# Kernel optimization log

Measured on AMD Instinct MI355X. Metric: run time of the kernel, lower is better.

Reference implementation:

```python
import jax, jax.numpy as jnp
from jax import lax
import numpy as np

SLOPE = 0.1  # LeakyReLU negative slope used throughout DA_conv


def setup_inputs() -> dict:
    key = jax.random.key(0)
    ks = jax.random.split(key, 8)
    B, C, H, W = 16, 64, 160, 160
    Cout, red = 64, 8
    feat = jax.random.normal(ks[0], (B, C, H, W), dtype=jnp.float32)
    deg = jax.random.normal(ks[1], (B, C, 1, 1), dtype=jnp.float32)
    W1 = jax.random.normal(ks[2], (64, C), dtype=jnp.float32) * 0.05
    W2 = jax.random.normal(ks[3], (Cout * 9, 64), dtype=jnp.float32) * 0.05
    Wc = jax.random.normal(ks[4], (Cout, Cout), dtype=jnp.float32) * 0.05
    bc = jnp.zeros((Cout,), dtype=jnp.float32)
    Wd1 = jax.random.normal(ks[5], (red, C), dtype=jnp.float32) * 0.05
    Wd2 = jax.random.normal(ks[6], (Cout, red), dtype=jnp.float32) * 0.05
    return {"feat": feat, "deg": deg, "W1": W1, "W2": W2, "Wc": Wc,
            "bc": bc, "Wd1": Wd1, "Wd2": Wd2}


def reference(feat, deg, W1, W2, Wc, bc, Wd1, Wd2):
    B, C, H, W = feat.shape
    Cout = Wc.shape[0]
    KS = 3
    d = deg[:, :, 0, 0]  # [B, C]

    # --- dynamic per-sample, per-channel 3x3 kernel generation ---
    h = jax.nn.leaky_relu(d @ W1.T, SLOPE)            # [B, 64]
    k = (h @ W2.T).reshape(B * Cout, 1, KS, KS)        # [B*Cout, 1, 3, 3]

    # grouped depthwise conv: input [1, B*C, H, W], groups = B*C
    x = feat.reshape(1, B * C, H, W)
    out = lax.conv_general_dilated(
        x, k, window_strides=(1, 1), padding=[(1, 1), (1, 1)],
        dimension_numbers=("NCHW", "OIHW", "NCHW"),
        feature_group_count=B * C)
    out = jax.nn.leaky_relu(out, SLOPE).reshape(B, Cout, H, W)

    # 1x1 conv with bias (common.default_conv)
    out = jnp.einsum("oi,bihw->bohw", Wc, out) + bc[None, :, None, None]

    # --- channel attention branch (1x1 convs == matmuls on [B,C]) ---
    a = jax.nn.leaky_relu(jnp.einsum("ri,bi->br", Wd1, d), SLOPE)   # [B, red]
    att = jax.nn.sigmoid(jnp.einsum("or,br->bo", Wd2, a))           # [B, Cout]

    return out + feat * att[:, :, None, None]
```

## Files before the change

### kernel.cpp

```cpp
#include <hip/hip_runtime.h>
#include <hip/hip_bf16.h>
#include <math.h>

#define SLOPE 0.1f
#define B_ 16
#define C_ 64
#define H_ 160
#define W_ 160
#define HW_ (H_*W_)

typedef short bf16x8 __attribute__((ext_vector_type(8)));
typedef float f32x4  __attribute__((ext_vector_type(4)));
typedef unsigned int uint2v __attribute__((ext_vector_type(2)));

__device__ __forceinline__ float lrelu(float x) { return fmaxf(x, SLOPE * x); }
__device__ __forceinline__ unsigned f2bf(float x) {
  union { float f; unsigned u; } c; c.f = x;
  return (c.u + 0x7fffu + ((c.u >> 16) & 1u)) >> 16;
}
__device__ __forceinline__ float bf2f(unsigned short u) {
  union { unsigned u; float f; } c; c.u = ((unsigned)u) << 16; return c.f;
}

__device__ __forceinline__ void gl2lds16(const void* g, void* l) {
  __builtin_amdgcn_global_load_lds(
      (const __attribute__((address_space(1))) void*)g,
      (__attribute__((address_space(3))) void*)l, 16, 0, 0);
}

__global__ __launch_bounds__(64) void prep_kernel(
    const float* __restrict__ deg,
    const float* __restrict__ W1,
    const float* __restrict__ W2,
    const float* __restrict__ Wd1,
    const float* __restrict__ Wd2,
    float* __restrict__ ws) {
  const int b = blockIdx.x;
  const int j = threadIdx.x;
  __shared__ float sd[64], sh[64], sa[8];
  sd[j] = deg[b * 64 + j];
  __syncthreads();

  float acc = 0.f;
  for (int i = 0; i < 64; ++i) acc = fmaf(sd[i], W1[j * 64 + i], acc);
  sh[j] = lrelu(acc);

  if (j < 8) {
    float s = 0.f;
    for (int i = 0; i < 64; ++i) s = fmaf(sd[i], Wd1[j * 64 + i], s);
    sa[j] = lrelu(s);
  }
  __syncthreads();

  float kv[9];
#pragma unroll
  for (int t = 0; t < 9; ++t) kv[t] = 0.f;
  for (int l = 0; l < 64; ++l) {
    float hl = sh[l];
#pragma unroll
    for (int t = 0; t < 9; ++t) kv[t] = fmaf(hl, W2[(j * 9 + t) * 64 + l], kv[t]);
  }
  unsigned short* kw = (unsigned short*)(ws + 1024) + (b * 64 + j) * 16;
#pragma unroll
  for (int t = 0; t < 9; ++t) kw[t] = (unsigned short)f2bf(kv[t]);
#pragma unroll
  for (int t = 9; t < 16; ++t) kw[t] = 0;

  float s2 = 0.f;
#pragma unroll
  for (int r = 0; r < 8; ++r) s2 = fmaf(Wd2[j * 8 + r], sa[r], s2);
  ws[b * 64 + j] = 1.f / (1.f + __expf(-s2));
}

__global__ __launch_bounds__(256, 4) void main_kernel(
    const float* __restrict__ feat,
    const float* __restrict__ Wc,
    const float* __restrict__ bc,
    const float* __restrict__ ws,
    float* __restrict__ out) {
  __shared__ __align__(16) float S[2][16][240];
  __shared__ __align__(16) unsigned short Tt[2048];
  __shared__ __align__(16) unsigned short Ff[2048];
  __shared__ __align__(16) unsigned short Kl[1024];

  const int rb  = blockIdx.x;
  const int bid = (rb & 7) * 400 + (rb >> 3);
  const int b   = bid / 200;
  const int rem = bid - b * 200;
  const int ty  = rem / 10, tx = rem - ty * 10;
  const int x0 = tx * 16, y0 = ty * 8;
  const int tid = threadIdx.x;
  const int lane = tid & 63, wid = tid >> 6;

  const float* __restrict__ attp  = ws + b * 64;
  const char*  __restrict__ kb8   = (const char*)(ws + 1024) + b * 2048;
  const float* __restrict__ plane = feat + (size_t)(b * 64) * HW_;

  const int ci = tid >> 4;
  const int q  = (tid >> 2) & 3;
  const int h  = tid & 3;
  const int nl = lane & 15, kg = lane >> 4;
  const int ochunk = wid * 16;

  const int srow = lane / 6;
  const int schk = lane - srow * 6;
  const int grow = min(max(y0 + srow - 1, 0), H_ - 1);
  const int gcol = min(max(x0 - 4 + schk * 4, 0), W_ - 4);
  const float* sp0 = plane + grow * W_ + gcol;

  union AF { bf16x8 v; unsigned short u[8]; };
  AF a[4];
#pragma unroll
  for (int g = 0; g < 4; ++g) {
    const float4 w = *(const float4*)(Wc + (ochunk + nl) * 64 + g * 16 + 4 * kg);
    a[g].u[0] = (unsigned short)f2bf(w.x); a[g].u[1] = (unsigned short)f2bf(w.y);
    a[g].u[2] = (unsigned short)f2bf(w.z); a[g].u[3] = (unsigned short)f2bf(w.w);
    a[g].u[4] = 0; a[g].u[5] = 0; a[g].u[6] = 0; a[g].u[7] = 0;
  }
  AF a2;
  {
    const unsigned short ab = (unsigned short)f2bf(attp[ochunk + nl]);
#pragma unroll
    for (int j = 0; j < 4; ++j) a2.u[j] = (nl == 4 * kg + j) ? ab : (unsigned short)0;
    a2.u[4] = 0; a2.u[5] = 0; a2.u[6] = 0; a2.u[7] = 0;
  }
  const float4 bcv = *(const float4*)(bc + ochunk + 4 * kg);

  asm volatile("s_waitcnt vmcnt(0)" ::: "memory");

  if (wid == 0) {
    gl2lds16(kb8 + lane * 16, &Kl[0]);
    gl2lds16(kb8 + 1024 + lane * 16, &Kl[512]);
  }
#define STAGE(g_, bf_) \
  if (lane < 60) { \
    const float* s_ = sp0 + (size_t)((g_) * 16 + wid * 4) * HW_; \
    gl2lds16(s_,            &S[bf_][wid * 4 + 0][0]); \
    gl2lds16(s_ + HW_,      &S[bf_][wid * 4 + 1][0]); \
    gl2lds16(s_ + 2 * HW_,  &S[bf_][wid * 4 + 2][0]); \
    gl2lds16(s_ + 3 * HW_,  &S[bf_][wid * 4 + 3][0]); \
  }
  STAGE(0, 0);
  asm volatile("s_waitcnt vmcnt(4)" ::: "memory");
  __builtin_amdgcn_s_barrier();
  __builtin_amdgcn_sched_barrier(0);

  f32x4 acc[8];
#pragma unroll
  for (int nt = 0; nt < 8; ++nt) acc[nt] = (f32x4){0.f, 0.f, 0.f, 0.f};

  const float mlz = (x0 == 0 && q == 0) ? 0.f : 1.f;
  const float mrz = (x0 == W_ - 16 && q == 3) ? 0.f : 1.f;

  const unsigned t_base = (unsigned)(uintptr_t)&Tt[0] + (unsigned)(lane * 8);
  const unsigned f_base = (unsigned)(uintptr_t)&Ff[0] + (unsigned)(lane * 8);
  union BU { bf16x8 v; uint2v qv[2]; };

#pragma unroll
  for (int g = 0; g < 4; ++g) {
    const int sb = g & 1;
    if (g < 3) {
      STAGE(g + 1, (g + 1) & 1);
      asm volatile("s_waitcnt vmcnt(4)" ::: "memory");
    } else {
      asm volatile("s_waitcnt vmcnt(0)" ::: "memory");
    }
    __builtin_amdgcn_sched_barrier(0);

    const unsigned short* kr = &Kl[(g * 16 + ci) * 16];
    union KU { uint4 v; unsigned short u[8]; } k07;
    k07.v = *(const uint4*)kr;
    const unsigned short k8u = kr[8];
    float kk[9];
#pragma unroll
    for (int t = 0; t < 8; ++t) kk[t] = bf2f(k07.u[t]);
    kk[8] = bf2f(k8u);

    float rv[4][9];
#pragma unroll
    for (int rr = 0; rr < 4; ++rr) {
      const float* sp = &S[sb][ci][(2 * h + rr) * 24 + 4 * q];
      const f32x4 v0 = *(const f32x4*)sp;
      const f32x4 v1 = *(const f32x4*)(sp + 4);
      rv[rr][0] = v0[0]; rv[rr][1] = v0[1]; rv[rr][2] = v0[2];
      rv[rr][3] = v0[3] * mlz;
      rv[rr][4] = v1[0]; rv[rr][5] = v1[1]; rv[rr][6] = v1[2]; rv[rr][7] = v1[3];
      rv[rr][8] = sp[8] * mrz;
    }

#pragma unroll
    for (int rr = 0; rr < 2; ++rr) {
      const int srw = 2 * h + rr;
      const float mt = (srw == 0 && y0 == 0) ? 0.f : 1.f;
      const float mb = (srw == 7 && y0 == H_ - 8) ? 0.f : 1.f;
      float sv[4], fv[4];
#pragma unroll
      for (int j = 0; j < 4; ++j) {
        float ts = fmaf(rv[rr][j + 5], kk[2], fmaf(rv[rr][j + 4], kk[1], rv[rr][j + 3] * kk[0]));
        float cs = fmaf(rv[rr + 1][j + 5], kk[5], fmaf(rv[rr + 1][j + 4], kk[4], rv[rr + 1][j + 3] * kk[3]));
        float bs = fmaf(rv[rr + 2][j + 5], kk[8], fmaf(rv[rr + 2][j + 4], kk[7], rv[rr + 2][j + 3] * kk[6]));
        sv[j] = fmaf(mt, ts, fmaf(mb, bs, cs));
        fv[j] = rv[rr + 1][j + 4];
      }
      uint2v tq, fq;
      tq.x = f2bf(lrelu(sv[0])) | (f2bf(lrelu(sv[1])) << 16);
      tq.y = f2bf(lrelu(sv[2])) | (f2bf(lrelu(sv[3])) << 16);
      fq.x = f2bf(fv[0]) | (f2bf(fv[1]) << 16);
      fq.y = f2bf(fv[2]) | (f2bf(fv[3]) << 16);
      const int tidx = srw * 256 + ci * 16 + 4 * q;
      *(uint2v*)&Tt[tidx] = tq;
      *(uint2v*)&Ff[tidx] = fq;
    }

    asm volatile("s_waitcnt lgkmcnt(0)" ::: "memory");
    __builtin_amdgcn_sched_barrier(0);
    __builtin_amdgcn_s_barrier();
    __builtin_amdgcn_sched_barrier(0);

    uint2v ta0, ta1, ta2, ta3, tb0, tb1, tb2, tb3;
    asm volatile("ds_read_b64_tr_b16 %0, %1 offset:0"    : "=v"(ta0) : "v"(t_base));
    asm volatile("ds_read_b64_tr_b16 %0, %1 offset:512"  : "=v"(ta1) : "v"(t_base));
    asm volatile("ds_read_b64_tr_b16 %0, %1 offset:1024" : "=v"(ta2) : "v"(t_base));
    asm volatile("ds_read_b64_tr_b16 %0, %1 offset:1536" : "=v"(ta3) : "v"(t_base));
    asm volatile("s_waitcnt lgkmcnt(0)" ::: "memory");
    __builtin_amdgcn_sched_barrier(0);
    asm volatile("ds_read_b64_tr_b16 %0, %1 offset:2048" : "=v"(tb0) : "v"(t_base));
    asm volatile("ds_read_b64_tr_b16 %0, %1 offset:2560" : "=v"(tb1) : "v"(t_base));
    asm volatile("ds_read_b64_tr_b16 %0, %1 offset:3072" : "=v"(tb2) : "v"(t_base));
    asm volatile("ds_read_b64_tr_b16 %0, %1 offset:3584" : "=v"(tb3) : "v"(t_base));
    {
      BU u0, u1, u2, u3;
      u0.qv[0] = ta0; u0.qv[1] = (uint2v){0u, 0u};
      u1.qv[0] = ta1; u1.qv[1] = (uint2v){0u, 0u};
      u2.qv[0] = ta2; u2.qv[1] = (uint2v){0u, 0u};
      u3.qv[0] = ta3; u3.qv[1] = (uint2v){0u, 0u};
      acc[0] = __builtin_amdgcn_mfma_f32_16x16x32_bf16(a[g].v, u0.v, acc[0], 0, 0, 0);
      acc[1] = __builtin_amdgcn_mfma_f32_16x16x32_bf16(a[g].v, u1.v, acc[1], 0, 0, 0);
      acc[2] = __builtin_amdgcn_mfma_f32_16x16x32_bf16(a[g].v, u2.v, acc[2], 0, 0, 0);
      acc[3] = __builtin_amdgcn_mfma_f32_16x16x32_bf16(a[g].v, u3.v, acc[3], 0, 0, 0);
    }
    asm volatile("s_waitcnt lgkmcnt(0)" ::: "memory");
    __builtin_amdgcn_sched_barrier(0);
    {
      BU u4, u5, u6, u7;
      u4.qv[0] = tb0; u4.qv[1] = (uint2v){0u, 0u};
      u5.qv[0] = tb1; u5.qv[1] = (uint2v){0u, 0u};
      u6.qv[0] = tb2; u6.qv[1] = (uint2v){0u, 0u};
      u7.qv[0] = tb3; u7.qv[1] = (uint2v){0u, 0u};
      acc[4] = __builtin_amdgcn_mfma_f32_16x16x32_bf16(a[g].v, u4.v, acc[4], 0, 0, 0);
      acc[5] = __builtin_amdgcn_mfma_f32_16x16x32_bf16(a[g].v, u5.v, acc[5], 0, 0, 0);
      acc[6] = __builtin_amdgcn_mfma_f32_16x16x32_bf16(a[g].v, u6.v, acc[6], 0, 0, 0);
      acc[7] = __builtin_amdgcn_mfma_f32_16x16x32_bf16(a[g].v, u7.v, acc[7], 0, 0, 0);
    }
    if (wid == g) {
      uint2v fa0, fa1, fa2, fa3, fb0, fb1, fb2, fb3;
      asm volatile("ds_read_b64_tr_b16 %0, %1 offset:0"    : "=v"(fa0) : "v"(f_base));
      asm volatile("ds_read_b64_tr_b16 %0, %1 offset:512"  : "=v"(fa1) : "v"(f_base));
      asm volatile("ds_read_b64_tr_b16 %0, %1 offset:1024" : "=v"(fa2) : "v"(f_base));
      asm volatile("ds_read_b64_tr_b16 %0, %1 offset:1536" : "=v"(fa3) : "v"(f_base));
      asm volatile("s_waitcnt lgkmcnt(0)" ::: "memory");
      __builtin_amdgcn_sched_barrier(0);
      asm volatile("ds_read_b64_tr_b16 %0, %1 offset:2048" : "=v"(fb0) : "v"(f_base));
      asm volatile("ds_read_b64_tr_b16 %0, %1 offset:2560" : "=v"(fb1) : "v"(f_base));
      asm volatile("ds_read_b64_tr_b16 %0, %1 offset:3072" : "=v"(fb2) : "v"(f_base));
      asm volatile("ds_read_b64_tr_b16 %0, %1 offset:3584" : "=v"(fb3) : "v"(f_base));
      {
        BU u0, u1, u2, u3;
        u0.qv[0] = fa0; u0.qv[1] = (uint2v){0u, 0u};
        u1.qv[0] = fa1; u1.qv[1] = (uint2v){0u, 0u};
        u2.qv[0] = fa2; u2.qv[1] = (uint2v){0u, 0u};
        u3.qv[0] = fa3; u3.qv[1] = (uint2v){0u, 0u};
        acc[0] = __builtin_amdgcn_mfma_f32_16x16x32_bf16(a2.v, u0.v, acc[0], 0, 0, 0);
        acc[1] = __builtin_amdgcn_mfma_f32_16x16x32_bf16(a2.v, u1.v, acc[1], 0, 0, 0);
        acc[2] = __builtin_amdgcn_mfma_f32_16x16x32_bf16(a2.v, u2.v, acc[2], 0, 0, 0);
        acc[3] = __builtin_amdgcn_mfma_f32_16x16x32_bf16(a2.v, u3.v, acc[3], 0, 0, 0);
      }
      asm volatile("s_waitcnt lgkmcnt(0)" ::: "memory");
      __builtin_amdgcn_sched_barrier(0);
      {
        BU u4, u5, u6, u7;
        u4.qv[0] = fb0; u4.qv[1] = (uint2v){0u, 0u};
        u5.qv[0] = fb1; u5.qv[1] = (uint2v){0u, 0u};
        u6.qv[0] = fb2; u6.qv[1] = (uint2v){0u, 0u};
        u7.qv[0] = fb3; u7.qv[1] = (uint2v){0u, 0u};
        acc[4] = __builtin_amdgcn_mfma_f32_16x16x32_bf16(a2.v, u4.v, acc[4], 0, 0, 0);
        acc[5] = __builtin_amdgcn_mfma_f32_16x16x32_bf16(a2.v, u5.v, acc[5], 0, 0, 0);
        acc[6] = __builtin_amdgcn_mfma_f32_16x16x32_bf16(a2.v, u6.v, acc[6], 0, 0, 0);
        acc[7] = __builtin_amdgcn_mfma_f32_16x16x32_bf16(a2.v, u7.v, acc[7], 0, 0, 0);
      }
    }
    __builtin_amdgcn_s_barrier();
    __builtin_amdgcn_sched_barrier(0);
  }
#undef STAGE

  const int ob = ochunk + 4 * kg;
  float* __restrict__ outb = out + (size_t)(b * 64) * HW_;
#pragma unroll
  for (int nt = 0; nt < 8; ++nt) {
    const int off = (y0 + nt) * W_ + x0 + nl;
    outb[(size_t)(ob + 0) * HW_ + off] = acc[nt][0] + bcv.x;
    outb[(size_t)(ob + 1) * HW_ + off] = acc[nt][1] + bcv.y;
    outb[(size_t)(ob + 2) * HW_ + off] = acc[nt][2] + bcv.z;
    outb[(size_t)(ob + 3) * HW_ + off] = acc[nt][3] + bcv.w;
  }
}

extern "C" void kernel_launch(void* const* d_in, const int* in_sizes, int n_in,
                              void* d_out, int out_size, void* d_ws, size_t ws_size,
                              hipStream_t stream) {
  const float* feat = (const float*)d_in[0];
  const float* deg  = (const float*)d_in[1];
  const float* W1   = (const float*)d_in[2];
  const float* W2   = (const float*)d_in[3];
  const float* Wc   = (const float*)d_in[4];
  const float* bc   = (const float*)d_in[5];
  const float* Wd1  = (const float*)d_in[6];
  const float* Wd2  = (const float*)d_in[7];
  float* out = (float*)d_out;
  float* ws  = (float*)d_ws;

  prep_kernel<<<dim3(B_), dim3(64), 0, stream>>>(deg, W1, W2, Wd1, Wd2, ws);
  main_kernel<<<dim3(3200), dim3(256), 0, stream>>>(feat, Wc, bc, ws, out);
}
```

Baseline: 67.30 us.

## Fold attention MFMA into main MFMA K-slot and deepen staging pipeline

Packs the attention-diagonal A fragment into the unused upper K half of each Wc fragment. The wave that owns the attention term for a group now issues one set of 8 MFMAs combining conv output and feature, not 16. Input staging is restructured so two groups are prefetched up front and the next-next group is issued after the LDS writes, removing the initial barrier. Dynamic-kernel weights are stored in a permuted slot order so all four waves load them cooperatively. This adds a tighter dependency between buffer reuse and the barrier, and interleaved ds_read waits.

```diff
diff --git a/kernel.cpp b/kernel.cpp
--- a/kernel.cpp
+++ b/kernel.cpp
@@ -60,7 +60,8 @@
 #pragma unroll
     for (int t = 0; t < 9; ++t) kv[t] = fmaf(hl, W2[(j * 9 + t) * 64 + l], kv[t]);
   }
-  unsigned short* kw = (unsigned short*)(ws + 1024) + (b * 64 + j) * 16;
+  const int slot = ((j & 15) >> 2) * 16 + (j >> 4) * 4 + (j & 3);
+  unsigned short* kw = (unsigned short*)(ws + 1024) + (b * 64 + slot) * 16;
 #pragma unroll
   for (int t = 0; t < 9; ++t) kw[t] = (unsigned short)f2bf(kv[t]);
 #pragma unroll
@@ -110,28 +111,21 @@
 
   union AF { bf16x8 v; unsigned short u[8]; };
   AF a[4];
+  const unsigned short ab = (unsigned short)f2bf(attp[ochunk + nl]);
 #pragma unroll
   for (int g = 0; g < 4; ++g) {
     const float4 w = *(const float4*)(Wc + (ochunk + nl) * 64 + g * 16 + 4 * kg);
     a[g].u[0] = (unsigned short)f2bf(w.x); a[g].u[1] = (unsigned short)f2bf(w.y);
     a[g].u[2] = (unsigned short)f2bf(w.z); a[g].u[3] = (unsigned short)f2bf(w.w);
-    a[g].u[4] = 0; a[g].u[5] = 0; a[g].u[6] = 0; a[g].u[7] = 0;
-  }
-  AF a2;
-  {
-    const unsigned short ab = (unsigned short)f2bf(attp[ochunk + nl]);
-#pragma unroll
-    for (int j = 0; j < 4; ++j) a2.u[j] = (nl == 4 * kg + j) ? ab : (unsigned short)0;
-    a2.u[4] = 0; a2.u[5] = 0; a2.u[6] = 0; a2.u[7] = 0;
+#pragma unroll
+    for (int j = 0; j < 4; ++j)
+      a[g].u[4 + j] = (wid == g && nl == 4 * kg + j) ? ab : (unsigned short)0;
   }
   const float4 bcv = *(const float4*)(bc + ochunk + 4 * kg);
 
   asm volatile("s_waitcnt vmcnt(0)" ::: "memory");
 
-  if (wid == 0) {
-    gl2lds16(kb8 + lane * 16, &Kl[0]);
-    gl2lds16(kb8 + 1024 + lane * 16, &Kl[512]);
-  }
+  if (lane < 32) gl2lds16(kb8 + wid * 512 + lane * 16, &Kl[wid * 256]);
 #define STAGE(g_, bf_) \
   if (lane < 60) { \
     const float* s_ = sp0 + (size_t)((g_) * 16 + wid * 4) * HW_; \
@@ -141,9 +135,7 @@
     gl2lds16(s_ + 3 * HW_,  &S[bf_][wid * 4 + 3][0]); \
   }
   STAGE(0, 0);
-  asm volatile("s_waitcnt vmcnt(4)" ::: "memory");
-  __builtin_amdgcn_s_barrier();
-  __builtin_amdgcn_sched_barrier(0);
+  STAGE(1, 1);
 
   f32x4 acc[8];
 #pragma unroll
@@ -160,14 +152,13 @@
   for (int g = 0; g < 4; ++g) {
     const int sb = g & 1;
     if (g < 3) {
-      STAGE(g + 1, (g + 1) & 1);
       asm volatile("s_waitcnt vmcnt(4)" ::: "memory");
     } else {
       asm volatile("s_waitcnt vmcnt(0)" ::: "memory");
     }
     __builtin_amdgcn_sched_barrier(0);
 
-    const unsigned short* kr = &Kl[(g * 16 + ci) * 16];
+    const unsigned short* kr = &Kl[(wid * 16 + g * 4 + (lane >> 4)) * 16];
     union KU { uint4 v; unsigned short u[8]; } k07;
     k07.v = *(const uint4*)kr;
     const unsigned short k8u = kr[8];
@@ -212,81 +203,103 @@
       *(uint2v*)&Ff[tidx] = fq;
     }
 
+    if (g < 2) { STAGE(g + 2, sb); }
+
     asm volatile("s_waitcnt lgkmcnt(0)" ::: "memory");
     __builtin_amdgcn_sched_barrier(0);
     __builtin_amdgcn_s_barrier();
     __builtin_amdgcn_sched_barrier(0);
 
-    uint2v ta0, ta1, ta2, ta3, tb0, tb1, tb2, tb3;
-    asm volatile("ds_read_b64_tr_b16 %0, %1 offset:0"    : "=v"(ta0) : "v"(t_base));
-    asm volatile("ds_read_b64_tr_b16 %0, %1 offset:512"  : "=v"(ta1) : "v"(t_base));
-    asm volatile("ds_read_b64_tr_b16 %0, %1 offset:1024" : "=v"(ta2) : "v"(t_base));
-    asm volatile("ds_read_b64_tr_b16 %0, %1 offset:1536" : "=v"(ta3) : "v"(t_base));
-    asm volatile("s_waitcnt lgkmcnt(0)" ::: "memory");
-    __builtin_amdgcn_sched_barrier(0);
-    asm volatile("ds_read_b64_tr_b16 %0, %1 offset:2048" : "=v"(tb0) : "v"(t_base));
-    asm volatile("ds_read_b64_tr_b16 %0, %1 offset:2560" : "=v"(tb1) : "v"(t_base));
-    asm volatile("ds_read_b64_tr_b16 %0, %1 offset:3072" : "=v"(tb2) : "v"(t_base));
-    asm volatile("ds_read_b64_tr_b16 %0, %1 offset:3584" : "=v"(tb3) : "v"(t_base));
-    {
-      BU u0, u1, u2, u3;
-      u0.qv[0] = ta0; u0.qv[1] = (uint2v){0u, 0u};
-      u1.qv[0] = ta1; u1.qv[1] = (uint2v){0u, 0u};
-      u2.qv[0] = ta2; u2.qv[1] = (uint2v){0u, 0u};
-      u3.qv[0] = ta3; u3.qv[1] = (uint2v){0u, 0u};
-      acc[0] = __builtin_amdgcn_mfma_f32_16x16x32_bf16(a[g].v, u0.v, acc[0], 0, 0, 0);
-      acc[1] = __builtin_amdgcn_mfma_f32_16x16x32_bf16(a[g].v, u1.v, acc[1], 0, 0, 0);
-      acc[2] = __builtin_amdgcn_mfma_f32_16x16x32_bf16(a[g].v, u2.v, acc[2], 0, 0, 0);
-      acc[3] = __builtin_amdgcn_mfma_f32_16x16x32_bf16(a[g].v, u3.v, acc[3], 0, 0, 0);
-    }
-    asm volatile("s_waitcnt lgkmcnt(0)" ::: "memory");
-    __builtin_amdgcn_sched_barrier(0);
-    {
-      BU u4, u5, u6, u7;
-      u4.qv[0] = tb0; u4.qv[1] = (uint2v){0u, 0u};
-      u5.qv[0] = tb1; u5.qv[1] = (uint2v){0u, 0u};
-      u6.qv[0] = tb2; u6.qv[1] = (uint2v){0u, 0u};
-      u7.qv[0] = tb3; u7.qv[1] = (uint2v){0u, 0u};
-      acc[4] = __builtin_amdgcn_mfma_f32_16x16x32_bf16(a[g].v, u4.v, acc[4], 0, 0, 0);
-      acc[5] = __builtin_amdgcn_mfma_f32_16x16x32_bf16(a[g].v, u5.v, acc[5], 0, 0, 0);
-      acc[6] = __builtin_amdgcn_mfma_f32_16x16x32_bf16(a[g].v, u6.v, acc[6], 0, 0, 0);
-      acc[7] = __builtin_amdgcn_mfma_f32_16x16x32_bf16(a[g].v, u7.v, acc[7], 0, 0, 0);
-    }
     if (wid == g) {
-      uint2v fa0, fa1, fa2, fa3, fb0, fb1, fb2, fb3;
-      asm volatile("ds_read_b64_tr_b16 %0, %1 offset:0"    : "=v"(fa0) : "v"(f_base));
-      asm volatile("ds_read_b64_tr_b16 %0, %1 offset:512"  : "=v"(fa1) : "v"(f_base));
-      asm volatile("ds_read_b64_tr_b16 %0, %1 offset:1024" : "=v"(fa2) : "v"(f_base));
-      asm volatile("ds_read_b64_tr_b16 %0, %1 offset:1536" : "=v"(fa3) : "v"(f_base));
+      uint2v t0, t1, t2, t3, t4, t5, t6, t7;
+      uint2v f0, f1, f2, f3, f4, f5, f6, f7;
+      asm volatile("ds_read_b64_tr_b16 %0, %1 offset:0"    : "=v"(t0) : "v"(t_base));
+      asm volatile("ds_read_b64_tr_b16 %0, %1 offset:512"  : "=v"(t1) : "v"(t_base));
+      asm volatile("ds_read_b64_tr_b16 %0, %1 offset:0"    : "=v"(f0) : "v"(f_base));
+      asm volatile("ds_read_b64_tr_b16 %0, %1 offset:512"  : "=v"(f1) : "v"(f_base));
+      asm volatile("ds_read_b64_tr_b16 %0, %1 offset:1024" : "=v"(t2) : "v"(t_base));
+      asm volatile("ds_read_b64_tr_b16 %0, %1 offset:1536" : "=v"(t3) : "v"(t_base));
+      asm volatile("ds_read_b64_tr_b16 %0, %1 offset:1024" : "=v"(f2) : "v"(f_base));
+      asm volatile("ds_read_b64_tr_b16 %0, %1 offset:1536" : "=v"(f3) : "v"(f_base));
+      asm volatile("s_waitcnt lgkmcnt(4)" ::: "memory");
+      __builtin_amdgcn_sched_barrier(0);
+      {
+        BU u0, u1;
+        u0.qv[0] = t0; u0.qv[1] = f0;
+        u1.qv[0] = t1; u1.qv[1] = f1;
+        acc[0] = __builtin_amdgcn_mfma_f32_16x16x32_bf16(a[g].v, u0.v, acc[0], 0, 0, 0);
+        acc[1] = __builtin_amdgcn_mfma_f32_16x16x32_bf16(a[g].v, u1.v, acc[1], 0, 0, 0);
+      }
+      asm volatile("ds_read_b64_tr_b16 %0, %1 offset:2048" : "=v"(t4) : "v"(t_base));
+      asm volatile("ds_read_b64_tr_b16 %0, %1 offset:2560" : "=v"(t5) : "v"(t_base));
+      asm volatile("ds_read_b64_tr_b16 %0, %1 offset:2048" : "=v"(f4) : "v"(f_base));
+      asm volatile("ds_read_b64_tr_b16 %0, %1 offset:2560" : "=v"(f5) : "v"(f_base));
+      asm volatile("s_waitcnt lgkmcnt(4)" ::: "memory");
+      __builtin_amdgcn_sched_barrier(0);
+      {
+        BU u2, u3;
+        u2.qv[0] = t2; u2.qv[1] = f2;
+        u3.qv[0] = t3; u3.qv[1] = f3;
+        acc[2] = __builtin_amdgcn_mfma_f32_16x16x32_bf16(a[g].v, u2.v, acc[2], 0, 0, 0);
+        acc[3] = __builtin_amdgcn_mfma_f32_16x16x32_bf16(a[g].v, u3.v, acc[3], 0, 0, 0);
+      }
+      asm volatile("ds_read_b64_tr_b16 %0, %1 offset:3072" : "=v"(t6) : "v"(t_base));
+      asm volatile("ds_read_b64_tr_b16 %0, %1 offset:3584" : "=v"(t7) : "v"(t_base));
+      asm volatile("ds_read_b64_tr_b16 %0, %1 offset:3072" : "=v"(f6) : "v"(f_base));
+      asm volatile("ds_read_b64_tr_b16 %0, %1 offset:3584" : "=v"(f7) : "v"(f_base));
+      asm volatile("s_waitcnt lgkmcnt(4)" ::: "memory");
+      __builtin_amdgcn_sched_barrier(0);
+      {
+        BU u4, u5;
+        u4.qv[0] = t4; u4.qv[1] = f4;
+        u5.qv[0] = t5; u5.qv[1] = f5;
+        acc[4] = __builtin_amdgcn_mfma_f32_16x16x32_bf16(a[g].v, u4.v, acc[4], 0, 0, 0);
+        acc[5] = __builtin_amdgcn_mfma_f32_16x16x32_bf16(a[g].v, u5.v, acc[5], 0, 0, 0);
+      }
       asm volatile("s_waitcnt lgkmcnt(0)" ::: "memory");
       __builtin_amdgcn_sched_barrier(0);
-      asm volatile("ds_read_b64_tr_b16 %0, %1 offset:2048" : "=v"(fb0) : "v"(f_base));
-      asm volatile("ds_read_b64_tr_b16 %0, %1 offset:2560" : "=v"(fb1) : "v"(f_base));
-      asm volatile("ds_read_b64_tr_b16 %0, %1 offset:3072" : "=v"(fb2) : "v"(f_base));
-      asm volatile("ds_read_b64_tr_b16 %0, %1 offset:3584" : "=v"(fb3) : "v"(f_base));
+      {
+        BU u6, u7;
+        u6.qv[0] = t6; u6.qv[1] = f6;
+        u7.qv[0] = t7; u7.qv[1] = f7;
+        acc[6] = __builtin_amdgcn_mfma_f32_16x16x32_bf16(a[g].v, u6.v, acc[6], 0, 0, 0);
+        acc[7] = __builtin_amdgcn_mfma_f32_16x16x32_bf16(a[g].v, u7.v, acc[7], 0, 0, 0);
+      }
+    } else {
+      uint2v ta0, ta1, ta2, ta3, tb0, tb1, tb2, tb3;
+      asm volatile("ds_read_b64_tr_b16 %0, %1 offset:0"    : "=v"(ta0) : "v"(t_base));
+      asm volatile("ds_read_b64_tr_b16 %0, %1 offset:512"  : "=v"(ta1) : "v"(t_base));
+      asm volatile("ds_read_b64_tr_b16 %0, %1 offset:1024" : "=v"(ta2) : "v"(t_base));
+      asm volatile("ds_read_b64_tr_b16 %0, %1 offset:1536" : "=v"(ta3) : "v"(t_base));
+      asm volatile("s_waitcnt lgkmcnt(0)" ::: "memory");
+      __builtin_amdgcn_sched_barrier(0);
+      asm volatile("ds_read_b64_tr_b16 %0, %1 offset:2048" : "=v"(tb0) : "v"(t_base));
+      asm volatile("ds_read_b64_tr_b16 %0, %1 offset:2560" : "=v"(tb1) : "v"(t_base));
+      asm volatile("ds_read_b64_tr_b16 %0, %1 offset:3072" : "=v"(tb2) : "v"(t_base));
+      asm volatile("ds_read_b64_tr_b16 %0, %1 offset:3584" : "=v"(tb3) : "v"(t_base));
       {
         BU u0, u1, u2, u3;
-        u0.qv[0] = fa0; u0.qv[1] = (uint2v){0u, 0u};
-        u1.qv[0] = fa1; u1.qv[1] = (uint2v){0u, 0u};
-        u2.qv[0] = fa2; u2.qv[1] = (uint2v){0u, 0u};
-        u3.qv[0] = fa3; u3.qv[1] = (uint2v){0u, 0u};
-        acc[0] = __builtin_amdgcn_mfma_f32_16x16x32_bf16(a2.v, u0.v, acc[0], 0, 0, 0);
-        acc[1] = __builtin_amdgcn_mfma_f32_16x16x32_bf16(a2.v, u1.v, acc[1], 0, 0, 0);
-        acc[2] = __builtin_amdgcn_mfma_f32_16x16x32_bf16(a2.v, u2.v, acc[2], 0, 0, 0);
-        acc[3] = __builtin_amdgcn_mfma_f32_16x16x32_bf16(a2.v, u3.v, acc[3], 0, 0, 0);
+        u0.qv[0] = ta0; u0.qv[1] = (uint2v){0u, 0u};
+        u1.qv[0] = ta1; u1.qv[1] = (uint2v){0u, 0u};
+        u2.qv[0] = ta2; u2.qv[1] = (uint2v){0u, 0u};
+        u3.qv[0] = ta3; u3.qv[1] = (uint2v){0u, 0u};
+        acc[0] = __builtin_amdgcn_mfma_f32_16x16x32_bf16(a[g].v, u0.v, acc[0], 0, 0, 0);
+        acc[1] = __builtin_amdgcn_mfma_f32_16x16x32_bf16(a[g].v, u1.v, acc[1], 0, 0, 0);
+        acc[2] = __builtin_amdgcn_mfma_f32_16x16x32_bf16(a[g].v, u2.v, acc[2], 0, 0, 0);
+        acc[3] = __builtin_amdgcn_mfma_f32_16x16x32_bf16(a[g].v, u3.v, acc[3], 0, 0, 0);
       }
       asm volatile("s_waitcnt lgkmcnt(0)" ::: "memory");
       __builtin_amdgcn_sched_barrier(0);
       {
         BU u4, u5, u6, u7;
-        u4.qv[0] = fb0; u4.qv[1] = (uint2v){0u, 0u};
-        u5.qv[0] = fb1; u5.qv[1] = (uint2v){0u, 0u};
-        u6.qv[0] = fb2; u6.qv[1] = (uint2v){0u, 0u};
-        u7.qv[0] = fb3; u7.qv[1] = (uint2v){0u, 0u};
-        acc[4] = __builtin_amdgcn_mfma_f32_16x16x32_bf16(a2.v, u4.v, acc[4], 0, 0, 0);
-        acc[5] = __builtin_amdgcn_mfma_f32_16x16x32_bf16(a2.v, u5.v, acc[5], 0, 0, 0);
-        acc[6] = __builtin_amdgcn_mfma_f32_16x16x32_bf16(a2.v, u6.v, acc[6], 0, 0, 0);
-        acc[7] = __builtin_amdgcn_mfma_f32_16x16x32_bf16(a2.v, u7.v, acc[7], 0, 0, 0);
+        u4.qv[0] = tb0; u4.qv[1] = (uint2v){0u, 0u};
+        u5.qv[0] = tb1; u5.qv[1] = (uint2v){0u, 0u};
+        u6.qv[0] = tb2; u6.qv[1] = (uint2v){0u, 0u};
+        u7.qv[0] = tb3; u7.qv[1] = (uint2v){0u, 0u};
+        acc[4] = __builtin_amdgcn_mfma_f32_16x16x32_bf16(a[g].v, u4.v, acc[4], 0, 0, 0);
+        acc[5] = __builtin_amdgcn_mfma_f32_16x16x32_bf16(a[g].v, u5.v, acc[5], 0, 0, 0);
+        acc[6] = __builtin_amdgcn_mfma_f32_16x16x32_bf16(a[g].v, u6.v, acc[6], 0, 0, 0);
+        acc[7] = __builtin_amdgcn_mfma_f32_16x16x32_bf16(a[g].v, u7.v, acc[7], 0, 0, 0);
       }
     }
     __builtin_amdgcn_s_barrier();
```

Measured after the change: 67.17 us. About the same (-0.2%).
